# Kernel tuning notes

Hardware: AMD Instinct MI355X
Metric: run time of the kernel (lower is better)

## Reference

```python
import jax, jax.numpy as jnp
import numpy as np

SEGMENT_LENGTHS = [1024, 2048, 4096]
DILATION_RATES = [1, 2, 4]


def _head_groups(num_heads, num_segments):
    base = num_heads // num_segments
    extra = num_heads % num_segments
    groups = [base] * num_segments
    for i in range(extra):
        groups[-(i + 1)] += 1
    return groups


def _dilated_indices(segment_len, dilation_rate, offset):
    # Mirrors RingDilatedAttentionV2._apply_dilation index construction (static).
    if dilation_rate > 1:
        idx = np.arange(offset, segment_len, dilation_rate)
        repeats = (segment_len + len(idx) - 1) // len(idx)
        idx = np.tile(idx, repeats)[:segment_len] % segment_len
    else:
        idx = np.arange(segment_len)
    return jnp.asarray(idx, dtype=jnp.int32)


def setup_inputs() -> dict:
    key = jax.random.key(0)
    kq, kk, kv = jax.random.split(key, 3)
    b, n, h, d = 1, 4096, 12, 64
    return {
        "query": jax.random.normal(kq, (b, n, h, d), dtype=jnp.float32),
        "key": jax.random.normal(kk, (b, n, h, d), dtype=jnp.float32),
        "value": jax.random.normal(kv, (b, n, h, d), dtype=jnp.float32),
        "is_causal": 1,
    }


def _dilated_attention(query, key, value, is_causal):
    b, n, h, d = query.shape
    groups = _head_groups(h, len(SEGMENT_LENGTHS))
    scale = 1.0 / np.sqrt(d).astype(np.float32)
    outs = []
    head_start = 0
    for i, (seg_len, rate, g) in enumerate(zip(SEGMENT_LENGTHS, DILATION_RATES, groups)):
        if g == 0:
            continue
        sl = min(seg_len, n)
        ns = n // sl  # n chosen divisible by every segment length
        q = query[:, :, head_start:head_start + g, :].reshape(b, ns, sl, g, d)
        k = key[:, :, head_start:head_start + g, :].reshape(b, ns, sl, g, d)
        v = value[:, :, head_start:head_start + g, :].reshape(b, ns, sl, g, d)
        if rate > 1 or i > 0:
            idx = _dilated_indices(sl, rate, i)
            k = k[:, :, idx]
            v = v[:, :, idx]
        # scores: [b, seg, heads, q_pos, k_pos]
        scores = jnp.einsum("bsqhd,bskhd->bshqk", q, k) * scale
        if is_causal:
            causal = jnp.triu(jnp.ones((sl, sl), dtype=bool), k=1)
            scores = jnp.where(causal, jnp.finfo(scores.dtype).min, scores)
        attn = jax.nn.softmax(scores, axis=-1)
        o = jnp.einsum("bshqk,bskhd->bsqhd", attn, v).reshape(b, n, g, d)
        outs.append(o)
        head_start += g
    return jnp.concatenate(outs, axis=2)  # [b, n, h, d]


def reference(query, key, value, is_causal):
    return _dilated_attention(query, key, value, is_causal)
```

## Files before the change

### kernel.cpp

```cpp
#include <hip/hip_runtime.h>
#include <hip/hip_bf16.h>
#include <math.h>

typedef __bf16 bf16x8 __attribute__((ext_vector_type(8)));
typedef float  f32x4  __attribute__((ext_vector_type(4)));
typedef unsigned short ushort_t;

#define LDK 72

#define KG_OFF  0
#define VGT_OFF 6291456
#define LACC_OFF 12582912

__device__ __forceinline__ int gather_pos(int gi, int group) {
    const int lsl = 10 + group;
    const int seg = gi >> lsl;
    const int j   = gi - (seg << lsl);
    return (seg << lsl) + group + ((j & 1023) << group);
}

__global__ __launch_bounds__(256)
void preconvert_kernel(const float* __restrict__ K, const float* __restrict__ V,
                       ushort_t* __restrict__ Kg, ushort_t* __restrict__ VgT)
{
    const int HD = 768;
    int b = blockIdx.x;
    const int tid = threadIdx.x;
    if (b < 768) {
        const int h = b % 12, gi0 = (b / 12) * 64;
        const int group = h >> 2;
        const int gi = gi0 + (tid >> 2);
        const int d0 = (tid & 3) << 4;
        const int pos = gather_pos(gi, group);
        const float* kp = K + (size_t)pos * HD + h * 64 + d0;
        float4 x0 = ((const float4*)kp)[0], x1 = ((const float4*)kp)[1];
        float4 x2 = ((const float4*)kp)[2], x3 = ((const float4*)kp)[3];
        bf16x8 w0, w1;
        w0[0]=(__bf16)x0.x; w0[1]=(__bf16)x0.y; w0[2]=(__bf16)x0.z; w0[3]=(__bf16)x0.w;
        w0[4]=(__bf16)x1.x; w0[5]=(__bf16)x1.y; w0[6]=(__bf16)x1.z; w0[7]=(__bf16)x1.w;
        w1[0]=(__bf16)x2.x; w1[1]=(__bf16)x2.y; w1[2]=(__bf16)x2.z; w1[3]=(__bf16)x2.w;
        w1[4]=(__bf16)x3.x; w1[5]=(__bf16)x3.y; w1[6]=(__bf16)x3.z; w1[7]=(__bf16)x3.w;
        ushort_t* out = Kg + ((size_t)(h * 4096 + gi)) * 64 + d0;
        *(bf16x8*)out = w0;
        *(bf16x8*)(out + 8) = w1;
    } else {
        b -= 768;
        const int h = b % 12, gi0 = (b / 12) * 64;
        const int group = h >> 2;
        __shared__ __align__(16) __bf16 Ts[64 * LDK];
        const int gil = tid >> 2;
        const int d0 = (tid & 3) << 4;
        const int pos = gather_pos(gi0 + gil, group);
        const float* vp = V + (size_t)pos * HD + h * 64 + d0;
        float4 x0 = ((const float4*)vp)[0], x1 = ((const float4*)vp)[1];
        float4 x2 = ((const float4*)vp)[2], x3 = ((const float4*)vp)[3];
        bf16x8 w0, w1;
        w0[0]=(__bf16)x0.x; w0[1]=(__bf16)x0.y; w0[2]=(__bf16)x0.z; w0[3]=(__bf16)x0.w;
        w0[4]=(__bf16)x1.x; w0[5]=(__bf16)x1.y; w0[6]=(__bf16)x1.z; w0[7]=(__bf16)x1.w;
        w1[0]=(__bf16)x2.x; w1[1]=(__bf16)x2.y; w1[2]=(__bf16)x2.z; w1[3]=(__bf16)x2.w;
        w1[4]=(__bf16)x3.x; w1[5]=(__bf16)x3.y; w1[6]=(__bf16)x3.z; w1[7]=(__bf16)x3.w;
        *(bf16x8*)&Ts[gil * LDK + d0]     = w0;
        *(bf16x8*)&Ts[gil * LDK + d0 + 8] = w1;
        __syncthreads();
        const int d = tid >> 2, c = tid & 3;
        bf16x8 o0, o1;
        #pragma unroll
        for (int i = 0; i < 8; ++i) {
            o0[i] = Ts[(c * 16 + i) * LDK + d];
            o1[i] = Ts[(c * 16 + 8 + i) * LDK + d];
        }
        ushort_t* out = VgT + ((size_t)(h * 64 + d)) * 4096 + gi0 + c * 16;
        *(bf16x8*)out = o0;
        *(bf16x8*)(out + 8) = o1;
    }
}

__global__ __launch_bounds__(256)
void dilated_attn_kernel(const float* __restrict__ Q,
                         const ushort_t* __restrict__ Kg,
                         const ushort_t* __restrict__ VgT,
                         const int* __restrict__ is_causal_p,
                         float* __restrict__ Out,
                         float* __restrict__ l_acc)
{
    const int HD = 768;
    const int bx  = blockIdx.x;
    const int qt  = 63 - (bx / 48);
    const int rem = bx % 48;
    const int h   = rem % 12;
    const int c   = rem / 12;
    const int group = h >> 2;
    const int sl    = 1024 << group;
    const int causal = (*is_causal_p) != 0;

    const int q0 = qt << 6;
    const int qb = q0 & (sl - 1);
    const int seg_start = q0 - qb;
    const int diag_kt = qb >> 6;
    const int nkt = causal ? (diag_kt + 1) : (sl >> 6);
    const int kt0 = c << 4;
    if (kt0 >= nkt) return;
    const int kend = min(kt0 + 16, nkt);
    const int nch  = (nkt + 15) >> 4;

    const int tid  = threadIdx.x;
    const int wave = tid >> 6;
    const int lane = tid & 63;
    const int l15  = lane & 15;
    const int quad = lane >> 4;

    __shared__ __align__(16) __bf16 Ks[2][64 * LDK];
    __shared__ __align__(16) __bf16 Vs[2][64 * LDK];
    __shared__ __align__(16) __bf16 Ps[4][16 * LDK];

    const int srow = tid >> 3;
    const int scol = (tid & 7) << 3;
    const ushort_t* kg_head = Kg + (size_t)h * 4096 * 64;
    const ushort_t* vt_head = VgT + (size_t)h * 64 * 4096;

    const int qrow = q0 + wave * 16 + l15;
    const float* qptr = Q + (size_t)qrow * HD + h * 64;
    bf16x8 a0, a1;
    {
        const float s = 0.125f * 1.4426950408889634f;
        float4 x0 = ((const float4*)(qptr + quad * 8))[0];
        float4 x1 = ((const float4*)(qptr + quad * 8))[1];
        float4 y0 = ((const float4*)(qptr + 32 + quad * 8))[0];
        float4 y1 = ((const float4*)(qptr + 32 + quad * 8))[1];
        a0[0]=(__bf16)(x0.x*s); a0[1]=(__bf16)(x0.y*s); a0[2]=(__bf16)(x0.z*s); a0[3]=(__bf16)(x0.w*s);
        a0[4]=(__bf16)(x1.x*s); a0[5]=(__bf16)(x1.y*s); a0[6]=(__bf16)(x1.z*s); a0[7]=(__bf16)(x1.w*s);
        a1[0]=(__bf16)(y0.x*s); a1[1]=(__bf16)(y0.y*s); a1[2]=(__bf16)(y0.z*s); a1[3]=(__bf16)(y0.w*s);
        a1[4]=(__bf16)(y1.x*s); a1[5]=(__bf16)(y1.y*s); a1[6]=(__bf16)(y1.z*s); a1[7]=(__bf16)(y1.w*s);
    }

    f32x4 o[4];
    #pragma unroll
    for (int t = 0; t < 4; ++t) o[t] = (f32x4){0.f, 0.f, 0.f, 0.f};
    float l_r[4] = {0.f, 0.f, 0.f, 0.f};

    bf16x8 kr0, kr1, vr0, vr1;
    auto load_tile = [&](int kt) {
        const ushort_t* kb = kg_head + (size_t)(seg_start + (kt << 6)) * 64;
        kr0 = *(const bf16x8*)(kb + srow * 64 + scol);
        kr1 = *(const bf16x8*)(kb + (srow + 32) * 64 + scol);
        const ushort_t* vb = vt_head + seg_start + (kt << 6);
        vr0 = *(const bf16x8*)(vb + (size_t)srow * 4096 + scol);
        vr1 = *(const bf16x8*)(vb + (size_t)(srow + 32) * 4096 + scol);
    };
    auto store_tile = [&](int buf) {
        *(bf16x8*)&Ks[buf][srow * LDK + scol]        = kr0;
        *(bf16x8*)&Ks[buf][(srow + 32) * LDK + scol] = kr1;
        *(bf16x8*)&Vs[buf][srow * LDK + scol]        = vr0;
        *(bf16x8*)&Vs[buf][(srow + 32) * LDK + scol] = vr1;
    };

    load_tile(kt0);
    store_tile(0);
    __syncthreads();

    for (int kt = kt0; kt < kend; ++kt) {
        const int cur = (kt - kt0) & 1;
        const bool more = (kt + 1 < kend);
        if (more) load_tile(kt + 1);

        f32x4 sacc[4];
        #pragma unroll
        for (int t = 0; t < 4; ++t) {
            bf16x8 b0 = *(const bf16x8*)&Ks[cur][(t * 16 + l15) * LDK + quad * 8];
            bf16x8 b1 = *(const bf16x8*)&Ks[cur][(t * 16 + l15) * LDK + 32 + quad * 8];
            f32x4 cc = (f32x4){0.f, 0.f, 0.f, 0.f};
            cc = __builtin_amdgcn_mfma_f32_16x16x32_bf16(a0, b0, cc, 0, 0, 0);
            cc = __builtin_amdgcn_mfma_f32_16x16x32_bf16(a1, b1, cc, 0, 0, 0);
            sacc[t] = cc;
        }

        const bool isdiag = causal && (kt == diag_kt);
        #pragma unroll
        for (int t = 0; t < 4; ++t) {
            const int col = t * 16 + l15;
            #pragma unroll
            for (int r = 0; r < 4; ++r) {
                const int row = wave * 16 + quad * 4 + r;
                float p = exp2f(sacc[t][r]);
                if (isdiag && col > row) p = 0.f;
                l_r[r] += p;
                Ps[wave][(quad * 4 + r) * LDK + t * 16 + l15] = (__bf16)p;
            }
        }

        bf16x8 p0 = *(const bf16x8*)&Ps[wave][l15 * LDK + quad * 8];
        bf16x8 p1 = *(const bf16x8*)&Ps[wave][l15 * LDK + 32 + quad * 8];
        #pragma unroll
        for (int t = 0; t < 4; ++t) {
            bf16x8 bv0 = *(const bf16x8*)&Vs[cur][(t * 16 + l15) * LDK + quad * 8];
            bf16x8 bv1 = *(const bf16x8*)&Vs[cur][(t * 16 + l15) * LDK + 32 + quad * 8];
            o[t] = __builtin_amdgcn_mfma_f32_16x16x32_bf16(p0, bv0, o[t], 0, 0, 0);
            o[t] = __builtin_amdgcn_mfma_f32_16x16x32_bf16(p1, bv1, o[t], 0, 0, 0);
        }

        if (more) store_tile(cur ^ 1);
        __syncthreads();
    }

    #pragma unroll
    for (int off = 1; off < 16; off <<= 1) {
        #pragma unroll
        for (int r = 0; r < 4; ++r)
            l_r[r] += __shfl_xor(l_r[r], off, 64);
    }
    if (nch == 1) {
        #pragma unroll
        for (int r = 0; r < 4; ++r) {
            const float inv = 1.0f / l_r[r];
            const int row = q0 + wave * 16 + quad * 4 + r;
            #pragma unroll
            for (int t = 0; t < 4; ++t)
                Out[(size_t)row * HD + h * 64 + t * 16 + l15] = o[t][r] * inv;
        }
    } else {
        #pragma unroll
        for (int r = 0; r < 4; ++r) {
            const int row = q0 + wave * 16 + quad * 4 + r;
            if (l15 == 0) atomicAdd(&l_acc[row * 12 + h], l_r[r]);
            #pragma unroll
            for (int t = 0; t < 4; ++t)
                atomicAdd(&Out[(size_t)row * HD + h * 64 + t * 16 + l15], o[t][r]);
        }
    }
}

__global__ __launch_bounds__(256)
void finalize_kernel(float* __restrict__ Out, const float* __restrict__ l_acc,
                     const int* __restrict__ is_causal_p)
{
    const int causal = (*is_causal_p) != 0;
    const int idx = blockIdx.x * 256 + threadIdx.x;
    const int rh = idx >> 4;
    const int d4 = idx & 15;
    const int h = rh % 12;
    const int row = rh / 12;
    const int group = h >> 2;
    const int ntf = 16 << group;
    const int qt = row >> 6;
    const int nkt = causal ? ((qt & (ntf - 1)) + 1) : ntf;
    if (nkt <= 16) return;
    const float inv = 1.0f / l_acc[rh];
    float4* p = (float4*)Out + (size_t)rh * 16 + d4;
    float4 v = *p;
    v.x *= inv; v.y *= inv; v.z *= inv; v.w *= inv;
    *p = v;
}

extern "C" void kernel_launch(void* const* d_in, const int* in_sizes, int n_in,
                              void* d_out, int out_size, void* d_ws, size_t ws_size,
                              hipStream_t stream) {
    (void)in_sizes; (void)n_in; (void)out_size; (void)ws_size;
    const float* Q = (const float*)d_in[0];
    const float* K = (const float*)d_in[1];
    const float* V = (const float*)d_in[2];
    const int* isc = (const int*)d_in[3];
    float* Out = (float*)d_out;
    ushort_t* Kg   = (ushort_t*)((char*)d_ws + KG_OFF);
    ushort_t* VgT  = (ushort_t*)((char*)d_ws + VGT_OFF);
    float*    lacc = (float*)((char*)d_ws + LACC_OFF);

    hipMemsetAsync(Out, 0, (size_t)4096 * 12 * 64 * 4, stream);
    hipMemsetAsync(lacc, 0, (size_t)4096 * 12 * 4, stream);
    preconvert_kernel<<<1536, 256, 0, stream>>>(K, V, Kg, VgT);
    dilated_attn_kernel<<<3072, 256, 0, stream>>>(Q, Kg, VgT, isc, Out, lacc);
    finalize_kernel<<<3072, 256, 0, stream>>>(Out, lacc, isc);
}
```

Baseline: 151.0 us.

## Double query tile to 128 rows per block, each wave handling 32 rows

Each block now processes 128 query rows instead of 64, with each wave computing two 16-row sub-tiles against the same K/V tiles in shared memory. This halves the number of K/V tile loads per query row and the grid size, amortizing global-to-LDS traffic over more MFMA work. In exchange, register use per thread roughly doubles for accumulators, and causal masking now spans two diagonal tiles, adding some wasted computation on masked entries. The finalize kernel's chunk-count logic is updated to match.

Result: slower. 166.8 us (+10.4%).

```diff
diff --git a/kernel.cpp b/kernel.cpp
--- a/kernel.cpp
+++ b/kernel.cpp
@@ -85,7 +85,7 @@
 {
     const int HD = 768;
     const int bx  = blockIdx.x;
-    const int qt  = 63 - (bx / 48);
+    const int qt  = 31 - (bx / 48);
     const int rem = bx % 48;
     const int h   = rem % 12;
     const int c   = rem / 12;
@@ -93,11 +93,11 @@
     const int sl    = 1024 << group;
     const int causal = (*is_causal_p) != 0;
 
-    const int q0 = qt << 6;
+    const int q0 = qt << 7;
     const int qb = q0 & (sl - 1);
     const int seg_start = q0 - qb;
-    const int diag_kt = qb >> 6;
-    const int nkt = causal ? (diag_kt + 1) : (sl >> 6);
+    const int diag0 = qb >> 6;
+    const int nkt = causal ? (diag0 + 2) : (sl >> 6);
     const int kt0 = c << 4;
     if (kt0 >= nkt) return;
     const int kend = min(kt0 + 16, nkt);
@@ -111,32 +111,41 @@
 
     __shared__ __align__(16) __bf16 Ks[2][64 * LDK];
     __shared__ __align__(16) __bf16 Vs[2][64 * LDK];
-    __shared__ __align__(16) __bf16 Ps[4][16 * LDK];
+    __shared__ __align__(16) __bf16 Ps[4][32 * LDK];
 
     const int srow = tid >> 3;
     const int scol = (tid & 7) << 3;
     const ushort_t* kg_head = Kg + (size_t)h * 4096 * 64;
     const ushort_t* vt_head = VgT + (size_t)h * 64 * 4096;
 
-    const int qrow = q0 + wave * 16 + l15;
-    const float* qptr = Q + (size_t)qrow * HD + h * 64;
-    bf16x8 a0, a1;
+    bf16x8 a[2][2];
     {
         const float s = 0.125f * 1.4426950408889634f;
-        float4 x0 = ((const float4*)(qptr + quad * 8))[0];
-        float4 x1 = ((const float4*)(qptr + quad * 8))[1];
-        float4 y0 = ((const float4*)(qptr + 32 + quad * 8))[0];
-        float4 y1 = ((const float4*)(qptr + 32 + quad * 8))[1];
-        a0[0]=(__bf16)(x0.x*s); a0[1]=(__bf16)(x0.y*s); a0[2]=(__bf16)(x0.z*s); a0[3]=(__bf16)(x0.w*s);
-        a0[4]=(__bf16)(x1.x*s); a0[5]=(__bf16)(x1.y*s); a0[6]=(__bf16)(x1.z*s); a0[7]=(__bf16)(x1.w*s);
-        a1[0]=(__bf16)(y0.x*s); a1[1]=(__bf16)(y0.y*s); a1[2]=(__bf16)(y0.z*s); a1[3]=(__bf16)(y0.w*s);
-        a1[4]=(__bf16)(y1.x*s); a1[5]=(__bf16)(y1.y*s); a1[6]=(__bf16)(y1.z*s); a1[7]=(__bf16)(y1.w*s);
-    }
-
-    f32x4 o[4];
+        #pragma unroll
+        for (int sub = 0; sub < 2; ++sub) {
+            const int qrow = q0 + wave * 32 + sub * 16 + l15;
+            const float* qptr = Q + (size_t)qrow * HD + h * 64;
+            float4 x0 = ((const float4*)(qptr + quad * 8))[0];
+            float4 x1 = ((const float4*)(qptr + quad * 8))[1];
+            float4 y0 = ((const float4*)(qptr + 32 + quad * 8))[0];
+            float4 y1 = ((const float4*)(qptr + 32 + quad * 8))[1];
+            a[sub][0][0]=(__bf16)(x0.x*s); a[sub][0][1]=(__bf16)(x0.y*s);
+            a[sub][0][2]=(__bf16)(x0.z*s); a[sub][0][3]=(__bf16)(x0.w*s);
+            a[sub][0][4]=(__bf16)(x1.x*s); a[sub][0][5]=(__bf16)(x1.y*s);
+            a[sub][0][6]=(__bf16)(x1.z*s); a[sub][0][7]=(__bf16)(x1.w*s);
+            a[sub][1][0]=(__bf16)(y0.x*s); a[sub][1][1]=(__bf16)(y0.y*s);
+            a[sub][1][2]=(__bf16)(y0.z*s); a[sub][1][3]=(__bf16)(y0.w*s);
+            a[sub][1][4]=(__bf16)(y1.x*s); a[sub][1][5]=(__bf16)(y1.y*s);
+            a[sub][1][6]=(__bf16)(y1.z*s); a[sub][1][7]=(__bf16)(y1.w*s);
+        }
+    }
+
+    f32x4 o[2][4];
     #pragma unroll
-    for (int t = 0; t < 4; ++t) o[t] = (f32x4){0.f, 0.f, 0.f, 0.f};
-    float l_r[4] = {0.f, 0.f, 0.f, 0.f};
+    for (int sub = 0; sub < 2; ++sub)
+        #pragma unroll
+        for (int t = 0; t < 4; ++t) o[sub][t] = (f32x4){0.f, 0.f, 0.f, 0.f};
+    float l_r[8] = {0.f,0.f,0.f,0.f,0.f,0.f,0.f,0.f};
 
     bf16x8 kr0, kr1, vr0, vr1;
     auto load_tile = [&](int kt) {
@@ -163,39 +172,52 @@
         const bool more = (kt + 1 < kend);
         if (more) load_tile(kt + 1);
 
-        f32x4 sacc[4];
+        f32x4 sacc[2][4];
         #pragma unroll
         for (int t = 0; t < 4; ++t) {
             bf16x8 b0 = *(const bf16x8*)&Ks[cur][(t * 16 + l15) * LDK + quad * 8];
             bf16x8 b1 = *(const bf16x8*)&Ks[cur][(t * 16 + l15) * LDK + 32 + quad * 8];
-            f32x4 cc = (f32x4){0.f, 0.f, 0.f, 0.f};
-            cc = __builtin_amdgcn_mfma_f32_16x16x32_bf16(a0, b0, cc, 0, 0, 0);
-            cc = __builtin_amdgcn_mfma_f32_16x16x32_bf16(a1, b1, cc, 0, 0, 0);
-            sacc[t] = cc;
-        }
-
-        const bool isdiag = causal && (kt == diag_kt);
-        #pragma unroll
-        for (int t = 0; t < 4; ++t) {
-            const int col = t * 16 + l15;
-            #pragma unroll
-            for (int r = 0; r < 4; ++r) {
-                const int row = wave * 16 + quad * 4 + r;
-                float p = exp2f(sacc[t][r]);
-                if (isdiag && col > row) p = 0.f;
-                l_r[r] += p;
-                Ps[wave][(quad * 4 + r) * LDK + t * 16 + l15] = (__bf16)p;
-            }
-        }
-
-        bf16x8 p0 = *(const bf16x8*)&Ps[wave][l15 * LDK + quad * 8];
-        bf16x8 p1 = *(const bf16x8*)&Ps[wave][l15 * LDK + 32 + quad * 8];
+            #pragma unroll
+            for (int sub = 0; sub < 2; ++sub) {
+                f32x4 cc = (f32x4){0.f, 0.f, 0.f, 0.f};
+                cc = __builtin_amdgcn_mfma_f32_16x16x32_bf16(a[sub][0], b0, cc, 0, 0, 0);
+                cc = __builtin_amdgcn_mfma_f32_16x16x32_bf16(a[sub][1], b1, cc, 0, 0, 0);
+                sacc[sub][t] = cc;
+            }
+        }
+
+        const bool maskTile = causal && (kt >= diag0);
+        #pragma unroll
+        for (int sub = 0; sub < 2; ++sub) {
+            #pragma unroll
+            for (int t = 0; t < 4; ++t) {
+                const int gcol = (kt << 6) + t * 16 + l15;
+                #pragma unroll
+                for (int r = 0; r < 4; ++r) {
+                    const int grow = qb + wave * 32 + sub * 16 + quad * 4 + r;
+                    float p = exp2f(sacc[sub][t][r]);
+                    if (maskTile && gcol > grow) p = 0.f;
+                    l_r[sub * 4 + r] += p;
+                    Ps[wave][(sub * 16 + quad * 4 + r) * LDK + t * 16 + l15] = (__bf16)p;
+                }
+            }
+        }
+
+        bf16x8 p0[2], p1[2];
+        #pragma unroll
+        for (int sub = 0; sub < 2; ++sub) {
+            p0[sub] = *(const bf16x8*)&Ps[wave][(sub * 16 + l15) * LDK + quad * 8];
+            p1[sub] = *(const bf16x8*)&Ps[wave][(sub * 16 + l15) * LDK + 32 + quad * 8];
+        }
         #pragma unroll
         for (int t = 0; t < 4; ++t) {
             bf16x8 bv0 = *(const bf16x8*)&Vs[cur][(t * 16 + l15) * LDK + quad * 8];
             bf16x8 bv1 = *(const bf16x8*)&Vs[cur][(t * 16 + l15) * LDK + 32 + quad * 8];
-            o[t] = __builtin_amdgcn_mfma_f32_16x16x32_bf16(p0, bv0, o[t], 0, 0, 0);
-            o[t] = __builtin_amdgcn_mfma_f32_16x16x32_bf16(p1, bv1, o[t], 0, 0, 0);
+            #pragma unroll
+            for (int sub = 0; sub < 2; ++sub) {
+                o[sub][t] = __builtin_amdgcn_mfma_f32_16x16x32_bf16(p0[sub], bv0, o[sub][t], 0, 0, 0);
+                o[sub][t] = __builtin_amdgcn_mfma_f32_16x16x32_bf16(p1[sub], bv1, o[sub][t], 0, 0, 0);
+            }
         }
 
         if (more) store_tile(cur ^ 1);
@@ -205,26 +227,32 @@
     #pragma unroll
     for (int off = 1; off < 16; off <<= 1) {
         #pragma unroll
-        for (int r = 0; r < 4; ++r)
-            l_r[r] += __shfl_xor(l_r[r], off, 64);
+        for (int i = 0; i < 8; ++i)
+            l_r[i] += __shfl_xor(l_r[i], off, 64);
     }
     if (nch == 1) {
         #pragma unroll
-        for (int r = 0; r < 4; ++r) {
-            const float inv = 1.0f / l_r[r];
-            const int row = q0 + wave * 16 + quad * 4 + r;
-            #pragma unroll
-            for (int t = 0; t < 4; ++t)
-                Out[(size_t)row * HD + h * 64 + t * 16 + l15] = o[t][r] * inv;
+        for (int sub = 0; sub < 2; ++sub) {
+            #pragma unroll
+            for (int r = 0; r < 4; ++r) {
+                const float inv = 1.0f / l_r[sub * 4 + r];
+                const int row = q0 + wave * 32 + sub * 16 + quad * 4 + r;
+                #pragma unroll
+                for (int t = 0; t < 4; ++t)
+                    Out[(size_t)row * HD + h * 64 + t * 16 + l15] = o[sub][t][r] * inv;
+            }
         }
     } else {
         #pragma unroll
-        for (int r = 0; r < 4; ++r) {
-            const int row = q0 + wave * 16 + quad * 4 + r;
-            if (l15 == 0) atomicAdd(&l_acc[row * 12 + h], l_r[r]);
-            #pragma unroll
-            for (int t = 0; t < 4; ++t)
-                atomicAdd(&Out[(size_t)row * HD + h * 64 + t * 16 + l15], o[t][r]);
+        for (int sub = 0; sub < 2; ++sub) {
+            #pragma unroll
+            for (int r = 0; r < 4; ++r) {
+                const int row = q0 + wave * 32 + sub * 16 + quad * 4 + r;
+                if (l15 == 0) atomicAdd(&l_acc[row * 12 + h], l_r[sub * 4 + r]);
+                #pragma unroll
+                for (int t = 0; t < 4; ++t)
+                    atomicAdd(&Out[(size_t)row * HD + h * 64 + t * 16 + l15], o[sub][t][r]);
+            }
         }
     }
 }
@@ -240,9 +268,10 @@
     const int h = rh % 12;
     const int row = rh / 12;
     const int group = h >> 2;
-    const int ntf = 16 << group;
-    const int qt = row >> 6;
-    const int nkt = causal ? ((qt & (ntf - 1)) + 1) : ntf;
+    const int sl = 1024 << group;
+    const int q0 = (row >> 7) << 7;
+    const int qb = q0 & (sl - 1);
+    const int nkt = causal ? ((qb >> 6) + 2) : (sl >> 6);
     if (nkt <= 16) return;
     const float inv = 1.0f / l_acc[rh];
     float4* p = (float4*)Out + (size_t)rh * 16 + d4;
@@ -267,6 +296,6 @@
     hipMemsetAsync(Out, 0, (size_t)4096 * 12 * 64 * 4, stream);
     hipMemsetAsync(lacc, 0, (size_t)4096 * 12 * 4, stream);
     preconvert_kernel<<<1536, 256, 0, stream>>>(K, V, Kg, VgT);
-    dilated_attn_kernel<<<3072, 256, 0, stream>>>(Q, Kg, VgT, isc, Out, lacc);
+    dilated_attn_kernel<<<1536, 256, 0, stream>>>(Q, Kg, VgT, isc, Out, lacc);
     finalize_kernel<<<3072, 256, 0, stream>>>(Out, lacc, isc);
 }
```

## Drop LDS staging: compute S^T with K as A-operand and pre-packed V fragments

Applied to the files above, without the earlier changes.

The attention kernel no longer stages K/V tiles through shared memory. It computes transposed scores (K as the MFMA A operand, Q as B) so probabilities land in registers already laid out as the B operand of the PV MFMA, which removes the P round-trip through LDS and all barriers. The preconvert kernel now writes V in an MFMA-fragment-packed layout so each lane loads its 8 values directly. Key chunks per block grow from 16 to 32 tiles, halving the grid and the atomic-reduction work, at the cost of less parallelism and global loads without double buffering.

After: 206.5 us. 36.7% more time.

```diff
diff --git a/kernel.cpp b/kernel.cpp
--- a/kernel.cpp
+++ b/kernel.cpp
@@ -9,7 +9,7 @@
 #define LDK 72
 
 #define KG_OFF  0
-#define VGT_OFF 6291456
+#define VP_OFF  6291456
 #define LACC_OFF 12582912
 
 __device__ __forceinline__ int gather_pos(int gi, int group) {
@@ -21,7 +21,7 @@
 
 __global__ __launch_bounds__(256)
 void preconvert_kernel(const float* __restrict__ K, const float* __restrict__ V,
-                       ushort_t* __restrict__ Kg, ushort_t* __restrict__ VgT)
+                       ushort_t* __restrict__ Kg, ushort_t* __restrict__ Vp)
 {
     const int HD = 768;
     int b = blockIdx.x;
@@ -45,15 +45,15 @@
         *(bf16x8*)(out + 8) = w1;
     } else {
         b -= 768;
-        const int h = b % 12, gi0 = (b / 12) * 64;
+        const int h = b % 12, kt = b / 12;
         const int group = h >> 2;
         __shared__ __align__(16) __bf16 Ts[64 * LDK];
         const int gil = tid >> 2;
         const int d0 = (tid & 3) << 4;
-        const int pos = gather_pos(gi0 + gil, group);
-        const float* vp = V + (size_t)pos * HD + h * 64 + d0;
-        float4 x0 = ((const float4*)vp)[0], x1 = ((const float4*)vp)[1];
-        float4 x2 = ((const float4*)vp)[2], x3 = ((const float4*)vp)[3];
+        const int pos = gather_pos(kt * 64 + gil, group);
+        const float* vpp = V + (size_t)pos * HD + h * 64 + d0;
+        float4 x0 = ((const float4*)vpp)[0], x1 = ((const float4*)vpp)[1];
+        float4 x2 = ((const float4*)vpp)[2], x3 = ((const float4*)vpp)[3];
         bf16x8 w0, w1;
         w0[0]=(__bf16)x0.x; w0[1]=(__bf16)x0.y; w0[2]=(__bf16)x0.z; w0[3]=(__bf16)x0.w;
         w0[4]=(__bf16)x1.x; w0[5]=(__bf16)x1.y; w0[6]=(__bf16)x1.z; w0[7]=(__bf16)x1.w;
@@ -62,31 +62,38 @@
         *(bf16x8*)&Ts[gil * LDK + d0]     = w0;
         *(bf16x8*)&Ts[gil * LDK + d0 + 8] = w1;
         __syncthreads();
-        const int d = tid >> 2, c = tid & 3;
-        bf16x8 o0, o1;
-        #pragma unroll
-        for (int i = 0; i < 8; ++i) {
-            o0[i] = Ts[(c * 16 + i) * LDK + d];
-            o1[i] = Ts[(c * 16 + 8 + i) * LDK + d];
-        }
-        ushort_t* out = VgT + ((size_t)(h * 64 + d)) * 4096 + gi0 + c * 16;
-        *(bf16x8*)out = o0;
-        *(bf16x8*)(out + 8) = o1;
+        ushort_t* vbase = Vp + ((size_t)(h * 64 + kt)) * 4096;
+        #pragma unroll
+        for (int u = 0; u < 2; ++u) {
+            const int c2 = tid * 2 + u;
+            const int kp2 = c2 >> 8;
+            const int t   = (c2 >> 6) & 3;
+            const int ln  = c2 & 63;
+            const int d   = t * 16 + (ln & 15);
+            const int kq  = (ln >> 4) << 2;
+            bf16x8 w;
+            #pragma unroll
+            for (int j = 0; j < 8; ++j) {
+                const int key_local = (kp2 * 2 + (j >> 2)) * 16 + kq + (j & 3);
+                w[j] = Ts[key_local * LDK + d];
+            }
+            *(bf16x8*)(vbase + (size_t)c2 * 8) = w;
+        }
     }
 }
 
 __global__ __launch_bounds__(256)
 void dilated_attn_kernel(const float* __restrict__ Q,
                          const ushort_t* __restrict__ Kg,
-                         const ushort_t* __restrict__ VgT,
+                         const ushort_t* __restrict__ Vp,
                          const int* __restrict__ is_causal_p,
                          float* __restrict__ Out,
                          float* __restrict__ l_acc)
 {
     const int HD = 768;
     const int bx  = blockIdx.x;
-    const int qt  = 63 - (bx / 48);
-    const int rem = bx % 48;
+    const int qt  = 63 - (bx / 24);
+    const int rem = bx % 24;
     const int h   = rem % 12;
     const int c   = rem / 12;
     const int group = h >> 2;
@@ -98,10 +105,10 @@
     const int seg_start = q0 - qb;
     const int diag_kt = qb >> 6;
     const int nkt = causal ? (diag_kt + 1) : (sl >> 6);
-    const int kt0 = c << 4;
+    const int kt0 = c << 5;
     if (kt0 >= nkt) return;
-    const int kend = min(kt0 + 16, nkt);
-    const int nch  = (nkt + 15) >> 4;
+    const int kend = min(kt0 + 32, nkt);
+    const int nch  = (nkt + 31) >> 5;
 
     const int tid  = threadIdx.x;
     const int wave = tid >> 6;
@@ -109,123 +116,87 @@
     const int l15  = lane & 15;
     const int quad = lane >> 4;
 
-    __shared__ __align__(16) __bf16 Ks[2][64 * LDK];
-    __shared__ __align__(16) __bf16 Vs[2][64 * LDK];
-    __shared__ __align__(16) __bf16 Ps[4][16 * LDK];
-
-    const int srow = tid >> 3;
-    const int scol = (tid & 7) << 3;
     const ushort_t* kg_head = Kg + (size_t)h * 4096 * 64;
-    const ushort_t* vt_head = VgT + (size_t)h * 64 * 4096;
-
-    const int qrow = q0 + wave * 16 + l15;
-    const float* qptr = Q + (size_t)qrow * HD + h * 64;
-    bf16x8 a0, a1;
+    const ushort_t* vp_head = Vp + (size_t)h * 64 * 4096;
+
+    bf16x8 bq0, bq1;
     {
         const float s = 0.125f * 1.4426950408889634f;
+        const int qrow = q0 + wave * 16 + l15;
+        const float* qptr = Q + (size_t)qrow * HD + h * 64;
         float4 x0 = ((const float4*)(qptr + quad * 8))[0];
         float4 x1 = ((const float4*)(qptr + quad * 8))[1];
         float4 y0 = ((const float4*)(qptr + 32 + quad * 8))[0];
         float4 y1 = ((const float4*)(qptr + 32 + quad * 8))[1];
-        a0[0]=(__bf16)(x0.x*s); a0[1]=(__bf16)(x0.y*s); a0[2]=(__bf16)(x0.z*s); a0[3]=(__bf16)(x0.w*s);
-        a0[4]=(__bf16)(x1.x*s); a0[5]=(__bf16)(x1.y*s); a0[6]=(__bf16)(x1.z*s); a0[7]=(__bf16)(x1.w*s);
-        a1[0]=(__bf16)(y0.x*s); a1[1]=(__bf16)(y0.y*s); a1[2]=(__bf16)(y0.z*s); a1[3]=(__bf16)(y0.w*s);
-        a1[4]=(__bf16)(y1.x*s); a1[5]=(__bf16)(y1.y*s); a1[6]=(__bf16)(y1.z*s); a1[7]=(__bf16)(y1.w*s);
+        bq0[0]=(__bf16)(x0.x*s); bq0[1]=(__bf16)(x0.y*s); bq0[2]=(__bf16)(x0.z*s); bq0[3]=(__bf16)(x0.w*s);
+        bq0[4]=(__bf16)(x1.x*s); bq0[5]=(__bf16)(x1.y*s); bq0[6]=(__bf16)(x1.z*s); bq0[7]=(__bf16)(x1.w*s);
+        bq1[0]=(__bf16)(y0.x*s); bq1[1]=(__bf16)(y0.y*s); bq1[2]=(__bf16)(y0.z*s); bq1[3]=(__bf16)(y0.w*s);
+        bq1[4]=(__bf16)(y1.x*s); bq1[5]=(__bf16)(y1.y*s); bq1[6]=(__bf16)(y1.z*s); bq1[7]=(__bf16)(y1.w*s);
     }
 
     f32x4 o[4];
     #pragma unroll
     for (int t = 0; t < 4; ++t) o[t] = (f32x4){0.f, 0.f, 0.f, 0.f};
-    float l_r[4] = {0.f, 0.f, 0.f, 0.f};
-
-    bf16x8 kr0, kr1, vr0, vr1;
-    auto load_tile = [&](int kt) {
+    float l_r = 0.f;
+    const int q_in_seg = qb + wave * 16 + l15;
+
+    for (int kt = kt0; kt < kend; ++kt) {
         const ushort_t* kb = kg_head + (size_t)(seg_start + (kt << 6)) * 64;
-        kr0 = *(const bf16x8*)(kb + srow * 64 + scol);
-        kr1 = *(const bf16x8*)(kb + (srow + 32) * 64 + scol);
-        const ushort_t* vb = vt_head + seg_start + (kt << 6);
-        vr0 = *(const bf16x8*)(vb + (size_t)srow * 4096 + scol);
-        vr1 = *(const bf16x8*)(vb + (size_t)(srow + 32) * 4096 + scol);
-    };
-    auto store_tile = [&](int buf) {
-        *(bf16x8*)&Ks[buf][srow * LDK + scol]        = kr0;
-        *(bf16x8*)&Ks[buf][(srow + 32) * LDK + scol] = kr1;
-        *(bf16x8*)&Vs[buf][srow * LDK + scol]        = vr0;
-        *(bf16x8*)&Vs[buf][(srow + 32) * LDK + scol] = vr1;
-    };
-
-    load_tile(kt0);
-    store_tile(0);
-    __syncthreads();
-
-    for (int kt = kt0; kt < kend; ++kt) {
-        const int cur = (kt - kt0) & 1;
-        const bool more = (kt + 1 < kend);
-        if (more) load_tile(kt + 1);
 
         f32x4 sacc[4];
         #pragma unroll
+        for (int kg = 0; kg < 4; ++kg) {
+            bf16x8 ka0 = *(const bf16x8*)(kb + (kg * 16 + l15) * 64 + quad * 8);
+            bf16x8 ka1 = *(const bf16x8*)(kb + (kg * 16 + l15) * 64 + 32 + quad * 8);
+            f32x4 cc = (f32x4){0.f, 0.f, 0.f, 0.f};
+            cc = __builtin_amdgcn_mfma_f32_16x16x32_bf16(ka0, bq0, cc, 0, 0, 0);
+            cc = __builtin_amdgcn_mfma_f32_16x16x32_bf16(ka1, bq1, cc, 0, 0, 0);
+            sacc[kg] = cc;
+        }
+
+        const bool maskT = causal && (kt == diag_kt);
+        bf16x8 pb[2];
+        #pragma unroll
+        for (int kg = 0; kg < 4; ++kg) {
+            #pragma unroll
+            for (int r = 0; r < 4; ++r) {
+                const int key = (kt << 6) + kg * 16 + quad * 4 + r;
+                float p = exp2f(sacc[kg][r]);
+                if (maskT && key > q_in_seg) p = 0.f;
+                l_r += p;
+                pb[kg >> 1][(kg & 1) * 4 + r] = (__bf16)p;
+            }
+        }
+
+        const ushort_t* vb = vp_head + (size_t)((seg_start >> 6) + kt) * 4096;
+        #pragma unroll
+        for (int kp2 = 0; kp2 < 2; ++kp2) {
+            #pragma unroll
+            for (int t = 0; t < 4; ++t) {
+                bf16x8 va = *(const bf16x8*)(vb + (size_t)(kp2 * 256 + t * 64 + lane) * 8);
+                o[t] = __builtin_amdgcn_mfma_f32_16x16x32_bf16(va, pb[kp2], o[t], 0, 0, 0);
+            }
+        }
+    }
+
+    l_r += __shfl_xor(l_r, 16, 64);
+    l_r += __shfl_xor(l_r, 32, 64);
+    const int row = q0 + wave * 16 + l15;
+    if (nch == 1) {
+        const float inv = 1.0f / l_r;
+        #pragma unroll
         for (int t = 0; t < 4; ++t) {
-            bf16x8 b0 = *(const bf16x8*)&Ks[cur][(t * 16 + l15) * LDK + quad * 8];
-            bf16x8 b1 = *(const bf16x8*)&Ks[cur][(t * 16 + l15) * LDK + 32 + quad * 8];
-            f32x4 cc = (f32x4){0.f, 0.f, 0.f, 0.f};
-            cc = __builtin_amdgcn_mfma_f32_16x16x32_bf16(a0, b0, cc, 0, 0, 0);
-            cc = __builtin_amdgcn_mfma_f32_16x16x32_bf16(a1, b1, cc, 0, 0, 0);
-            sacc[t] = cc;
-        }
-
-        const bool isdiag = causal && (kt == diag_kt);
-        #pragma unroll
-        for (int t = 0; t < 4; ++t) {
-            const int col = t * 16 + l15;
-            #pragma unroll
-            for (int r = 0; r < 4; ++r) {
-                const int row = wave * 16 + quad * 4 + r;
-                float p = exp2f(sacc[t][r]);
-                if (isdiag && col > row) p = 0.f;
-                l_r[r] += p;
-                Ps[wave][(quad * 4 + r) * LDK + t * 16 + l15] = (__bf16)p;
-            }
-        }
-
-        bf16x8 p0 = *(const bf16x8*)&Ps[wave][l15 * LDK + quad * 8];
-        bf16x8 p1 = *(const bf16x8*)&Ps[wave][l15 * LDK + 32 + quad * 8];
-        #pragma unroll
-        for (int t = 0; t < 4; ++t) {
-            bf16x8 bv0 = *(const bf16x8*)&Vs[cur][(t * 16 + l15) * LDK + quad * 8];
-            bf16x8 bv1 = *(const bf16x8*)&Vs[cur][(t * 16 + l15) * LDK + 32 + quad * 8];
-            o[t] = __builtin_amdgcn_mfma_f32_16x16x32_bf16(p0, bv0, o[t], 0, 0, 0);
-            o[t] = __builtin_amdgcn_mfma_f32_16x16x32_bf16(p1, bv1, o[t], 0, 0, 0);
-        }
-
-        if (more) store_tile(cur ^ 1);
-        __syncthreads();
-    }
-
-    #pragma unroll
-    for (int off = 1; off < 16; off <<= 1) {
-        #pragma unroll
-        for (int r = 0; r < 4; ++r)
-            l_r[r] += __shfl_xor(l_r[r], off, 64);
-    }
-    if (nch == 1) {
-        #pragma unroll
-        for (int r = 0; r < 4; ++r) {
-            const float inv = 1.0f / l_r[r];
-            const int row = q0 + wave * 16 + quad * 4 + r;
-            #pragma unroll
-            for (int t = 0; t < 4; ++t)
-                Out[(size_t)row * HD + h * 64 + t * 16 + l15] = o[t][r] * inv;
+            f32x4 v = o[t];
+            float4 w = {v[0] * inv, v[1] * inv, v[2] * inv, v[3] * inv};
+            *(float4*)(Out + (size_t)row * HD + h * 64 + t * 16 + quad * 4) = w;
         }
     } else {
-        #pragma unroll
-        for (int r = 0; r < 4; ++r) {
-            const int row = q0 + wave * 16 + quad * 4 + r;
-            if (l15 == 0) atomicAdd(&l_acc[row * 12 + h], l_r[r]);
-            #pragma unroll
-            for (int t = 0; t < 4; ++t)
-                atomicAdd(&Out[(size_t)row * HD + h * 64 + t * 16 + l15], o[t][r]);
-        }
+        if (lane < 16) atomicAdd(&l_acc[row * 12 + h], l_r);
+        #pragma unroll
+        for (int t = 0; t < 4; ++t)
+            #pragma unroll
+            for (int r = 0; r < 4; ++r)
+                atomicAdd(&Out[(size_t)row * HD + h * 64 + t * 16 + quad * 4 + r], o[t][r]);
     }
 }
 
@@ -240,10 +211,11 @@
     const int h = rh % 12;
     const int row = rh / 12;
     const int group = h >> 2;
-    const int ntf = 16 << group;
-    const int qt = row >> 6;
-    const int nkt = causal ? ((qt & (ntf - 1)) + 1) : ntf;
-    if (nkt <= 16) return;
+    const int sl = 1024 << group;
+    const int q0 = row & ~63;
+    const int qb = q0 & (sl - 1);
+    const int nkt = causal ? ((qb >> 6) + 1) : (sl >> 6);
+    if (nkt <= 32) return;
     const float inv = 1.0f / l_acc[rh];
     float4* p = (float4*)Out + (size_t)rh * 16 + d4;
     float4 v = *p;
@@ -261,12 +233,12 @@
     const int* isc = (const int*)d_in[3];
     float* Out = (float*)d_out;
     ushort_t* Kg   = (ushort_t*)((char*)d_ws + KG_OFF);
-    ushort_t* VgT  = (ushort_t*)((char*)d_ws + VGT_OFF);
+    ushort_t* Vp   = (ushort_t*)((char*)d_ws + VP_OFF);
     float*    lacc = (float*)((char*)d_ws + LACC_OFF);
 
     hipMemsetAsync(Out, 0, (size_t)4096 * 12 * 64 * 4, stream);
     hipMemsetAsync(lacc, 0, (size_t)4096 * 12 * 4, stream);
-    preconvert_kernel<<<1536, 256, 0, stream>>>(K, V, Kg, VgT);
-    dilated_attn_kernel<<<3072, 256, 0, stream>>>(Q, Kg, VgT, isc, Out, lacc);
+    preconvert_kernel<<<1536, 256, 0, stream>>>(K, V, Kg, Vp);
+    dilated_attn_kernel<<<1536, 256, 0, stream>>>(Q, Kg, Vp, isc, Out, lacc);
     finalize_kernel<<<3072, 256, 0, stream>>>(Out, lacc, isc);
 }
```
